# Optimization experiments

Hardware: AMD Instinct MI355X
Metric: run time of the kernel (lower is better)

Reference implementation:

```python
import jax, jax.numpy as jnp
import numpy as np

BN_EPS = 1e-5
POOL_TARGETS = (1500, 750, 375)


def mesh_conv(x, nb, W, g, b):
    # x: (E, C), nb: (E, 4), W: (5*C, Cout)
    E, C = x.shape
    n = x[jnp.clip(nb, 0, E - 1)]              # (E, 4, C) gather
    p1 = jnp.sort(n[:, :2, :], axis=1)          # symmetrize face-pair 1
    p2 = jnp.sort(n[:, 2:, :], axis=1)          # symmetrize face-pair 2
    feat = jnp.concatenate([x, p1[:, 0], p1[:, 1], p2[:, 0], p2[:, 1]], axis=1)  # (E, 5C)
    h = feat @ W                                # (E, Cout)
    mu = h.mean(axis=0)
    var = h.var(axis=0)                         # biased var (BatchNorm training stats)
    h = (h - mu) * jax.lax.rsqrt(var + BN_EPS) * g + b
    return jax.nn.relu(h)


def mesh_pool(x, nb, target):
    E = x.shape[0]
    scores = jnp.linalg.norm(x, axis=1)
    keep = jnp.sort(jnp.argsort(-scores)[:target])          # (target,) sorted kept edges
    x_pool = x[keep]
    remap = jnp.full((E,), -1, dtype=jnp.int32).at[keep].set(jnp.arange(target, dtype=jnp.int32))
    nbr = remap[jnp.clip(nb[keep], 0, E - 1)]               # (target, 4)
    self_idx = jnp.broadcast_to(jnp.arange(target, dtype=jnp.int32)[:, None], nbr.shape)
    nb_pool = jnp.where(nbr < 0, self_idx, nbr)
    return x_pool, nb_pool, keep


def mesh_unpool(x_coarse, keep, E_fine):
    # keep is sorted ascending; nearest kept edge by integer index distance
    # (ties -> lower index, matching torch argmin-first semantics).
    idx = jnp.arange(E_fine)
    pos = jnp.searchsorted(keep, idx)
    K = keep.shape[0]
    left = jnp.clip(pos - 1, 0, K - 1)
    right = jnp.clip(pos, 0, K - 1)
    dl = jnp.abs(idx - keep[left])
    dr = jnp.abs(idx - keep[right])
    nn_idx = jnp.where(dl <= dr, left, right)
    return x_coarse[nn_idx]                                 # kept edges map to themselves (d=0)


def setup_inputs() -> dict:
    key = jax.random.key(0)
    ks = jax.random.split(key, 20)
    E = 200000
    x = jax.random.normal(ks[0], (E, 5), dtype=jnp.float32)
    nb = jax.random.randint(ks[1], (E, 4), 0, E, dtype=jnp.int64)

    def lin(k, cin, cout):
        return (jax.random.normal(k, (cin, cout), dtype=jnp.float32) * 0.05)

    dims = [(5, 64), (64, 128), (128, 256), (256, 512), (768, 256), (384, 128), (192, 64)]
    names = ['e1', 'e2', 'e3', 'e4', 'd3', 'd2', 'd1']
    inp = {'x': x, 'nb': nb}
    for i, ((cin, cout), nm) in enumerate(zip(dims, names)):
        inp['W_' + nm] = lin(ks[2 + i], cin * 5, cout)
        inp['g_' + nm] = jnp.ones((cout,), dtype=jnp.float32)
        inp['b_' + nm] = jnp.zeros((cout,), dtype=jnp.float32)
    inp['W_head'] = lin(ks[12], 64, 4)
    inp['bias_head'] = jnp.zeros((4,), dtype=jnp.float32)
    return inp


def _forward(x, nb,
             W_e1, g_e1, b_e1, W_e2, g_e2, b_e2, W_e3, g_e3, b_e3, W_e4, g_e4, b_e4,
             W_d3, g_d3, b_d3, W_d2, g_d2, b_d2, W_d1, g_d1, b_d1,
             W_head, bias_head):
    e1 = mesh_conv(x, nb, W_e1, g_e1, b_e1)
    e1p, nb1, keep1 = mesh_pool(e1, nb, POOL_TARGETS[0])
    e2 = mesh_conv(e1p, nb1, W_e2, g_e2, b_e2)
    e2p, nb2, keep2 = mesh_pool(e2, nb1, POOL_TARGETS[1])
    e3 = mesh_conv(e2p, nb2, W_e3, g_e3, b_e3)
    e3p, nb3, keep3 = mesh_pool(e3, nb2, POOL_TARGETS[2])
    e4 = mesh_conv(e3p, nb3, W_e4, g_e4, b_e4)
    d3 = mesh_unpool(e4, keep3, e3.shape[0])
    d3 = mesh_conv(jnp.concatenate([d3, e3], axis=1), nb2, W_d3, g_d3, b_d3)
    d2 = mesh_unpool(d3, keep2, e2.shape[0])
    d2 = mesh_conv(jnp.concatenate([d2, e2], axis=1), nb1, W_d2, g_d2, b_d2)
    d1 = mesh_unpool(d2, keep1, e1.shape[0])
    d1 = mesh_conv(jnp.concatenate([d1, e1], axis=1), nb, W_d1, g_d1, b_d1)
    return d1 @ W_head + bias_head


def reference(x, nb,
              W_e1, g_e1, b_e1, W_e2, g_e2, b_e2, W_e3, g_e3, b_e3, W_e4, g_e4, b_e4,
              W_d3, g_d3, b_d3, W_d2, g_d2, b_d2, W_d1, g_d1, b_d1,
              W_head, bias_head):
    return _forward(x, nb,
                    W_e1, g_e1, b_e1, W_e2, g_e2, b_e2, W_e3, g_e3, b_e3, W_e4, g_e4, b_e4,
                    W_d3, g_d3, b_d3, W_d2, g_d2, b_d2, W_d1, g_d1, b_d1,
                    W_head, bias_head)
```

## Files before the change

kernel.cpp:

```cpp
#include <hip/hip_runtime.h>
#include <stdint.h>

typedef unsigned long long u64;
typedef unsigned int u32;
typedef unsigned short ushort_t;

#define FI __device__ __forceinline__

static constexpr float BN_EPS_F = 1e-5f;
static constexpr int E0 = 200000;
static constexpr int T1 = 1500, T2 = 750, T3 = 375;
static constexpr int CAND_CAP = 4096;
static constexpr int NB_KEEP = (E0 + 1023) / 1024;

typedef __attribute__((ext_vector_type(8))) short short8;
typedef __attribute__((ext_vector_type(4))) float f32x4;

FI int iclampi(int v, int lo, int hi) { return v < lo ? lo : (v > hi ? hi : v); }

FI ushort_t f2b(float f) {
  u32 u = __float_as_uint(f);
  u32 r = (u + 0x7FFFu + ((u >> 16) & 1u)) >> 16;
  return (ushort_t)r;
}

FI void u16minmax(const uint4& va, const uint4& vb, uint4& lo, uint4& hi) {
  const ushort_t* a = (const ushort_t*)&va;
  const ushort_t* b = (const ushort_t*)&vb;
  ushort_t* l = (ushort_t*)&lo;
  ushort_t* h = (ushort_t*)&hi;
  #pragma unroll
  for (int i = 0; i < 8; i++) {
    ushort_t x = a[i], y = b[i];
    l[i] = x < y ? x : y;
    h[i] = x < y ? y : x;
  }
}

FI int nearest_keep(const int* __restrict__ keep, int K, int idx) {
  int lo = 0, hi = K;
  while (lo < hi) { int mid = (lo + hi) >> 1; if (keep[mid] < idx) lo = mid + 1; else hi = mid; }
  int l = lo - 1; l = l < 0 ? 0 : (l > K - 1 ? K - 1 : l);
  int r = lo;     r = r < 0 ? 0 : (r > K - 1 ? K - 1 : r);
  int dl = idx - keep[l]; dl = dl < 0 ? -dl : dl;
  int dr = idx - keep[r]; dr = dr < 0 ? -dr : dr;
  return (dl <= dr) ? l : r;
}

FI int bsearch_eq(const int* __restrict__ keep, int K, int v) {
  int lo = 0, hi = K;
  while (lo < hi) { int mid = (lo + hi) >> 1; if (keep[mid] < v) lo = mid + 1; else hi = mid; }
  if (lo < K && keep[lo] == v) return lo;
  return -1;
}

template<int C, int Cout, int BR, int BC, int KT, int TR, int TC, int KSPLIT,
         bool FUSE_STATS>
__global__ __launch_bounds__((BR / TR) * (BC / TC))
void conv_kernel(const float* __restrict__ X,
                 const int* __restrict__ nb, int E,
                 const float* __restrict__ W,
                 float* __restrict__ H, float* __restrict__ stats)
{
  constexpr int NTH = (BR / TR) * (BC / TC);
  constexpr int VK = 5 * KT;
  constexpr int KC = C / KSPLIT;
  static_assert(KC % KT == 0, "KC % KT");

  const int row0 = blockIdx.x * BR;
  const int col0 = blockIdx.y * BC;
  const int c_begin = (KSPLIT > 1) ? (int)blockIdx.z * KC : 0;

  __shared__ float As[VK][BR];
  __shared__ float Bs[VK][BC];
  __shared__ int rowsS[5][BR];
  __shared__ float red[FUSE_STATS ? 2 * (BR / TR) * BC : 1];

  const int tid = threadIdx.x;

  for (int q = tid; q < BR; q += NTH) {
    int r = row0 + q;
    int rr[5];
    if (r < E) {
      rr[0] = r;
      #pragma unroll
      for (int j = 0; j < 4; j++) {
        int v = nb[(size_t)r * 4 + j];
        rr[1 + j] = iclampi(v, 0, E - 1);
      }
    } else {
      #pragma unroll
      for (int j = 0; j < 5; j++) rr[j] = -1;
    }
    #pragma unroll
    for (int j = 0; j < 5; j++) rowsS[j][q] = rr[j];
  }

  float acc[TR][TC];
  #pragma unroll
  for (int i = 0; i < TR; i++)
    #pragma unroll
    for (int j = 0; j < TC; j++) acc[i][j] = 0.f;

  const int tr = tid / (BC / TC);
  const int tc = tid % (BC / TC);
  const int rA = tr * TR;
  const int cB = tc * TC;

  for (int c0 = c_begin; c0 < c_begin + KC; c0 += KT) {
    __syncthreads();
    for (int q = tid; q < VK * (BC / 4); q += NTH) {
      int kk = q / (BC / 4);
      int c4 = q % (BC / 4);
      int p = kk / KT, t = kk % KT;
      float4 wv = *(const float4*)&W[(size_t)(p * C + c0 + t) * Cout + col0 + c4 * 4];
      *(float4*)&Bs[kk][c4 * 4] = wv;
    }
    for (int q = tid; q < BR * KT; q += NTH) {
      int t = q % KT, rq = q / KT;
      int c = c0 + t;
      float s0 = 0.f, a1 = 0.f, a2 = 0.f, a3 = 0.f, a4 = 0.f;
      if (rowsS[0][rq] >= 0) {
        float v0, v1, v2, v3;
        s0 = X[(size_t)rowsS[0][rq] * C + c];
        v0 = X[(size_t)rowsS[1][rq] * C + c];
        v1 = X[(size_t)rowsS[2][rq] * C + c];
        v2 = X[(size_t)rowsS[3][rq] * C + c];
        v3 = X[(size_t)rowsS[4][rq] * C + c];
        a1 = fminf(v0, v1); a2 = fmaxf(v0, v1);
        a3 = fminf(v2, v3); a4 = fmaxf(v2, v3);
      }
      As[0 * KT + t][rq] = s0;
      As[1 * KT + t][rq] = a1;
      As[2 * KT + t][rq] = a2;
      As[3 * KT + t][rq] = a3;
      As[4 * KT + t][rq] = a4;
    }
    __syncthreads();

    for (int kk = 0; kk < VK; kk++) {
      float a[TR], b[TC];
      #pragma unroll
      for (int i = 0; i < TR; i++) a[i] = As[kk][rA + i];
      #pragma unroll
      for (int j = 0; j < TC; j++) b[j] = Bs[kk][cB + j];
      #pragma unroll
      for (int i = 0; i < TR; i++)
        #pragma unroll
        for (int j = 0; j < TC; j++)
          acc[i][j] = fmaf(a[i], b[j], acc[i][j]);
    }
  }

  #pragma unroll
  for (int i = 0; i < TR; i++) {
    int r = row0 + rA + i;
    if (r < E) {
      if constexpr (KSPLIT > 1) {
        #pragma unroll
        for (int j = 0; j < TC; j++)
          atomicAdd(&H[(size_t)r * Cout + col0 + cB + j], acc[i][j]);
      } else {
        #pragma unroll
        for (int j = 0; j < TC; j += 4) {
          float4 v = make_float4(acc[i][j], acc[i][j + 1], acc[i][j + 2], acc[i][j + 3]);
          *(float4*)&H[(size_t)r * Cout + col0 + cB + j] = v;
        }
      }
    }
  }

  if constexpr (FUSE_STATS) {
    float s[TC], q2[TC];
    #pragma unroll
    for (int j = 0; j < TC; j++) { s[j] = 0.f; q2[j] = 0.f; }
    #pragma unroll
    for (int i = 0; i < TR; i++) {
      int r = row0 + rA + i;
      if (r < E) {
        #pragma unroll
        for (int j = 0; j < TC; j++) { float v = acc[i][j]; s[j] += v; q2[j] += v * v; }
      }
    }
    __syncthreads();
    float* redS = &red[0];
    float* redQ = &red[(BR / TR) * BC];
    #pragma unroll
    for (int j = 0; j < TC; j++) {
      redS[tr * BC + cB + j] = s[j];
      redQ[tr * BC + cB + j] = q2[j];
    }
    __syncthreads();
    for (int col = tid; col < BC; col += NTH) {
      float ts = 0.f, tq = 0.f;
      for (int g = 0; g < BR / TR; g++) { ts += redS[g * BC + col]; tq += redQ[g * BC + col]; }
      atomicAdd(&stats[col0 + col], ts);
      atomicAdd(&stats[Cout + col0 + col], tq);
    }
  }
}

__global__ __launch_bounds__(256)
void e1_conv_kernel(const float* __restrict__ X, const int* __restrict__ nb,
                    const float* __restrict__ W,
                    float* __restrict__ H, float* __restrict__ stats)
{
  __shared__ float As[25][128];
  __shared__ float Bs[25][64];
  __shared__ float red[2 * 32 * 64];

  const int tid = threadIdx.x;
  const int row0 = (int)blockIdx.x * 128;

  if (tid < 128) {
    int r = row0 + tid; if (r > E0 - 1) r = E0 - 1;
    int rs[5];
    rs[0] = r;
    #pragma unroll
    for (int j = 0; j < 4; j++) rs[1 + j] = iclampi((int)nb[(size_t)r * 4 + j], 0, E0 - 1);
    float v[5][5];
    #pragma unroll
    for (int j = 0; j < 5; j++) {
      const float* src = &X[(size_t)rs[j] * 5];
      float4 a = *(const float4*)src;
      v[j][0] = a.x; v[j][1] = a.y; v[j][2] = a.z; v[j][3] = a.w;
      v[j][4] = src[4];
    }
    #pragma unroll
    for (int c = 0; c < 5; c++) {
      As[0 * 5 + c][tid] = v[0][c];
      As[1 * 5 + c][tid] = fminf(v[1][c], v[2][c]);
      As[2 * 5 + c][tid] = fmaxf(v[1][c], v[2][c]);
      As[3 * 5 + c][tid] = fminf(v[3][c], v[4][c]);
      As[4 * 5 + c][tid] = fmaxf(v[3][c], v[4][c]);
    }
  } else {
    for (int q = tid - 128; q < 25 * 16; q += 128) {
      int k = q / 16, c4 = q % 16;
      float4 wv = *(const float4*)&W[(size_t)k * 64 + c4 * 4];
      *(float4*)&Bs[k][c4 * 4] = wv;
    }
  }
  __syncthreads();

  const int tr = tid >> 3;
  const int tc = tid & 7;
  const int rA = tr * 4;
  const int cB = tc * 8;

  float acc[4][8];
  #pragma unroll
  for (int i = 0; i < 4; i++)
    #pragma unroll
    for (int j = 0; j < 8; j++) acc[i][j] = 0.f;

  for (int k = 0; k < 25; k++) {
    float a[4], b[8];
    #pragma unroll
    for (int i = 0; i < 4; i++) a[i] = As[k][rA + i];
    #pragma unroll
    for (int j = 0; j < 8; j++) b[j] = Bs[k][cB + j];
    #pragma unroll
    for (int i = 0; i < 4; i++)
      #pragma unroll
      for (int j = 0; j < 8; j++)
        acc[i][j] = fmaf(a[i], b[j], acc[i][j]);
  }

  float s[8], q2[8];
  #pragma unroll
  for (int j = 0; j < 8; j++) { s[j] = 0.f; q2[j] = 0.f; }
  #pragma unroll
  for (int i = 0; i < 4; i++) {
    int r = row0 + rA + i;
    if (r < E0) {
      #pragma unroll
      for (int j = 0; j < 8; j += 4) {
        float4 v = make_float4(acc[i][j], acc[i][j + 1], acc[i][j + 2], acc[i][j + 3]);
        *(float4*)&H[(size_t)r * 64 + cB + j] = v;
      }
      #pragma unroll
      for (int j = 0; j < 8; j++) { float v = acc[i][j]; s[j] += v; q2[j] += v * v; }
    }
  }
  __syncthreads();
  float* redS = &red[0];
  float* redQ = &red[32 * 64];
  #pragma unroll
  for (int j = 0; j < 8; j++) {
    redS[tr * 64 + cB + j] = s[j];
    redQ[tr * 64 + cB + j] = q2[j];
  }
  __syncthreads();
  for (int col = tid; col < 64; col += 256) {
    float ts = 0.f, tq = 0.f;
    for (int g = 0; g < 32; g++) { ts += redS[g * 64 + col]; tq += redQ[g * 64 + col]; }
    atomicAdd(&stats[col], ts);
    atomicAdd(&stats[64 + col], tq);
  }
}

template<int C, int Cout>
__global__ __launch_bounds__(128)
void mfma_conv_kernel(const ushort_t* __restrict__ src,
                      const int* __restrict__ nb, int E,
                      const ushort_t* __restrict__ Wt,
                      float* __restrict__ H, float* __restrict__ stats)
{
  constexpr int NCC = C / 32;
  __shared__ int rows[5][32];

  const int tid = threadIdx.x;
  const int lane = tid & 63;
  const int wv = tid >> 6;
  const int l15 = lane & 15;
  const int quad = lane >> 4;
  const int row0 = (int)blockIdx.x * 32;
  const int col0 = (int)blockIdx.y * 64;

  if (tid < 32) {
    int r = row0 + tid; if (r > E - 1) r = E - 1;
    rows[0][tid] = r;
    #pragma unroll
    for (int j = 0; j < 4; j++) rows[1 + j][tid] = iclampi(nb[(size_t)r * 4 + j], 0, E - 1);
  }
  __syncthreads();

  const int rr = wv * 16 + l15;
  int r5[5];
  #pragma unroll
  for (int j = 0; j < 5; j++) r5[j] = rows[j][rr];

  f32x4 acc[4];
  #pragma unroll
  for (int ni = 0; ni < 4; ni++) acc[ni] = (f32x4){0.f, 0.f, 0.f, 0.f};

  uint4 raw[2][5];
  auto loadcc = [&](int par, int cc2) {
    int cb = cc2 * 32 + quad * 8;
    #pragma unroll
    for (int j = 0; j < 5; j++)
      raw[par][j] = *(const uint4*)&src[(size_t)r5[j] * C + cb];
  };

  loadcc(0, 0);
  #pragma unroll
  for (int cc = 0; cc < NCC; cc++) {
    const int par = cc & 1;
    if (cc + 1 < NCC) loadcc(par ^ 1, cc + 1);
    short8 a[5];
    a[0] = *(short8*)&raw[par][0];
    {
      uint4 lo, hi;
      u16minmax(raw[par][1], raw[par][2], lo, hi);
      a[1] = *(short8*)&lo; a[2] = *(short8*)&hi;
    }
    {
      uint4 lo, hi;
      u16minmax(raw[par][3], raw[par][4], lo, hi);
      a[3] = *(short8*)&lo; a[4] = *(short8*)&hi;
    }
    #pragma unroll
    for (int p = 0; p < 5; p++) {
      #pragma unroll
      for (int ni = 0; ni < 4; ni++) {
        short8 bf = *(const short8*)&Wt[((size_t)(p * Cout + col0 + ni * 16 + l15)) * C + cc * 32 + quad * 8];
        acc[ni] = __builtin_amdgcn_mfma_f32_16x16x32_bf16(a[p], bf, acc[ni], 0, 0, 0);
      }
    }
  }

  float s[4] = {0.f, 0.f, 0.f, 0.f}, q[4] = {0.f, 0.f, 0.f, 0.f};
  #pragma unroll
  for (int reg = 0; reg < 4; reg++) {
    int r = row0 + wv * 16 + quad * 4 + reg;
    if (r < E) {
      #pragma unroll
      for (int ni = 0; ni < 4; ni++) {
        float v = acc[ni][reg];
        H[(size_t)r * Cout + col0 + ni * 16 + l15] = v;
        s[ni] += v; q[ni] += v * v;
      }
    }
  }
  #pragma unroll
  for (int ni = 0; ni < 4; ni++) {
    float ts = s[ni], tq = q[ni];
    ts += __shfl_xor(ts, 16); tq += __shfl_xor(tq, 16);
    ts += __shfl_xor(ts, 32); tq += __shfl_xor(tq, 32);
    if (quad == 0) {
      int col = col0 + ni * 16 + l15;
      atomicAdd(&stats[col], ts);
      atomicAdd(&stats[Cout + col], tq);
    }
  }
}

__global__ __launch_bounds__(256, 2)
void d1_mfma_kernel(const ushort_t* __restrict__ d2b, const ushort_t* __restrict__ e1b,
                    const int* __restrict__ nn1, const int* __restrict__ nb,
                    const ushort_t* __restrict__ Wt,
                    float* __restrict__ H, float* __restrict__ stats)
{
  __shared__ int rowsD[5][128];
  __shared__ int rowsS[5][128];

  const int tid = threadIdx.x;
  const int lane = tid & 63;
  const int wv = tid >> 6;
  const int l15 = lane & 15;
  const int quad = lane >> 4;
  const int row0 = (int)blockIdx.x * 128;

  if (tid < 128) {
    int r = row0 + tid; if (r > E0 - 1) r = E0 - 1;
    int rs[5];
    rs[0] = r;
    #pragma unroll
    for (int j = 0; j < 4; j++) rs[1 + j] = iclampi((int)nb[(size_t)r * 4 + j], 0, E0 - 1);
    #pragma unroll
    for (int j = 0; j < 5; j++) { rowsS[j][tid] = rs[j]; rowsD[j][tid] = nn1[rs[j]]; }
  }
  __syncthreads();

  int rD[2][5], rS[2][5];
  #pragma unroll
  for (int mi = 0; mi < 2; mi++) {
    int rr = wv * 32 + mi * 16 + l15;
    #pragma unroll
    for (int j = 0; j < 5; j++) { rD[mi][j] = rowsD[j][rr]; rS[mi][j] = rowsS[j][rr]; }
  }

  f32x4 acc[2][4];
  #pragma unroll
  for (int mi = 0; mi < 2; mi++)
    #pragma unroll
    for (int ni = 0; ni < 4; ni++) acc[mi][ni] = (f32x4){0.f, 0.f, 0.f, 0.f};

  uint4 raw[2][2][5];
  auto loadcc = [&](int par, int cc2) {
    const bool fD = cc2 < 4;
    const ushort_t* s2 = fD ? d2b : e1b;
    const int st = fD ? 128 : 64;
    const int cb = (fD ? cc2 * 32 : (cc2 - 4) * 32) + quad * 8;
    #pragma unroll
    for (int mi = 0; mi < 2; mi++)
      #pragma unroll
      for (int j = 0; j < 5; j++) {
        int r = fD ? rD[mi][j] : rS[mi][j];
        raw[par][mi][j] = *(const uint4*)&s2[(size_t)r * st + cb];
      }
  };

  loadcc(0, 0);
  #pragma unroll
  for (int cc = 0; cc < 6; cc++) {
    const int par = cc & 1;
    if (cc + 1 < 6) loadcc(par ^ 1, cc + 1);
    short8 a[2][5];
    #pragma unroll
    for (int mi = 0; mi < 2; mi++) {
      a[mi][0] = *(short8*)&raw[par][mi][0];
      {
        uint4 lo, hi;
        u16minmax(raw[par][mi][1], raw[par][mi][2], lo, hi);
        a[mi][1] = *(short8*)&lo; a[mi][2] = *(short8*)&hi;
      }
      {
        uint4 lo, hi;
        u16minmax(raw[par][mi][3], raw[par][mi][4], lo, hi);
        a[mi][3] = *(short8*)&lo; a[mi][4] = *(short8*)&hi;
      }
    }
    #pragma unroll
    for (int p = 0; p < 5; p++) {
      short8 bf[4];
      #pragma unroll
      for (int ni = 0; ni < 4; ni++)
        bf[ni] = *(const short8*)&Wt[((size_t)(p * 64 + ni * 16 + l15)) * 192 + cc * 32 + quad * 8];
      #pragma unroll
      for (int mi = 0; mi < 2; mi++)
        #pragma unroll
        for (int ni = 0; ni < 4; ni++)
          acc[mi][ni] = __builtin_amdgcn_mfma_f32_16x16x32_bf16(a[mi][p], bf[ni], acc[mi][ni], 0, 0, 0);
    }
  }

  float s[4] = {0.f, 0.f, 0.f, 0.f}, q[4] = {0.f, 0.f, 0.f, 0.f};
  #pragma unroll
  for (int mi = 0; mi < 2; mi++) {
    #pragma unroll
    for (int reg = 0; reg < 4; reg++) {
      int r = row0 + wv * 32 + mi * 16 + quad * 4 + reg;
      if (r < E0) {
        #pragma unroll
        for (int ni = 0; ni < 4; ni++) {
          float v = acc[mi][ni][reg];
          H[(size_t)r * 64 + ni * 16 + l15] = v;
          s[ni] += v; q[ni] += v * v;
        }
      }
    }
  }
  #pragma unroll
  for (int ni = 0; ni < 4; ni++) {
    float ts = s[ni], tq = q[ni];
    ts += __shfl_xor(ts, 16); tq += __shfl_xor(tq, 16);
    ts += __shfl_xor(ts, 32); tq += __shfl_xor(tq, 32);
    if (quad == 0) {
      int col = ni * 16 + l15;
      atomicAdd(&stats[col], ts);
      atomicAdd(&stats[64 + col], tq);
    }
  }
}

template<int C, int Cout>
__global__ void prep_w_kernel(const float* __restrict__ W, ushort_t* __restrict__ Wt)
{
  int idx = (int)blockIdx.x * 256 + threadIdx.x;
  if (idx < 5 * C * Cout) {
    int n = idx % Cout;
    int k = idx / Cout;
    int p = k / C, c = k % C;
    Wt[((size_t)(p * Cout + n)) * C + c] = f2b(W[(size_t)k * Cout + n]);
  }
}

__global__ void stats_kernel(const float* __restrict__ H, int E, int Cout,
                             float* __restrict__ stats)
{
  const int RB = 64;
  int r0 = (int)blockIdx.x * RB;
  int rend = r0 + RB; if (rend > E) rend = E;
  for (int col = threadIdx.x; col < Cout; col += blockDim.x) {
    float s = 0.f, q = 0.f;
    for (int r = r0; r < rend; r++) { float v = H[(size_t)r * Cout + col]; s += v; q += v * v; }
    atomicAdd(&stats[col], s);
    atomicAdd(&stats[Cout + col], q);
  }
}

template<int Cout, bool KEYS, bool B16>
__global__ void bn_kernel(const float* __restrict__ H, const float* __restrict__ stats,
                          const float* __restrict__ g, const float* __restrict__ b,
                          int E, float* __restrict__ Out, ushort_t* __restrict__ Outb,
                          u64* __restrict__ keys)
{
  constexpr int CPL = Cout / 64;
  const int lane = threadIdx.x & 63;
  const int wid = threadIdx.x >> 6;
  const int wpb = blockDim.x >> 6;
  const float invE = 1.0f / (float)E;
  float mu[CPL], inv[CPL], gg[CPL], bb[CPL];
  #pragma unroll
  for (int u = 0; u < CPL; u++) {
    int c = lane + u * 64;
    float m = stats[c] * invE;
    float var = stats[Cout + c] * invE - m * m;
    mu[u] = m;
    inv[u] = rsqrtf(var + BN_EPS_F);
    gg[u] = g[c]; bb[u] = b[c];
  }
  for (int r = (int)blockIdx.x * wpb + wid; r < E; r += (int)gridDim.x * wpb) {
    float ss = 0.f;
    #pragma unroll
    for (int u = 0; u < CPL; u++) {
      int c = lane + u * 64;
      float v = H[(size_t)r * Cout + c];
      float o = (v - mu[u]) * inv[u] * gg[u] + bb[u];
      o = fmaxf(o, 0.f);
      Out[(size_t)r * Cout + c] = o;
      if constexpr (B16) Outb[(size_t)r * Cout + c] = f2b(o);
      ss += o * o;
    }
    if constexpr (KEYS) {
      #pragma unroll
      for (int s = 32; s > 0; s >>= 1) ss += __shfl_xor(ss, s, 64);
      if (lane == 0) {
        float sc = sqrtf(ss);
        u32 sb = __float_as_uint(sc);
        keys[r] = ((u64)sb << 32) | (u64)(0xFFFFFFFFu - (u32)r);
      }
    }
  }
}

__global__ void head_kernel(const float* __restrict__ H, const float* __restrict__ stats,
                            const float* __restrict__ g, const float* __restrict__ b,
                            const float* __restrict__ Wh, const float* __restrict__ bh,
                            int E, float* __restrict__ out)
{
  const int lane = threadIdx.x & 63;
  const int wid = threadIdx.x >> 6;
  const int wpb = blockDim.x >> 6;
  const float invE = 1.0f / (float)E;
  float m = stats[lane] * invE;
  float var = stats[64 + lane] * invE - m * m;
  float inv = rsqrtf(var + BN_EPS_F);
  float gg = g[lane], bb = b[lane];
  float4 w = *(const float4*)&Wh[lane * 4];
  float b0 = bh[0], b1 = bh[1], b2 = bh[2], b3 = bh[3];
  for (int r = (int)blockIdx.x * wpb + wid; r < E; r += (int)gridDim.x * wpb) {
    float v = H[(size_t)r * 64 + lane];
    float o = fmaxf((v - m) * inv * gg + bb, 0.f);
    float a0 = o * w.x, a1 = o * w.y, a2 = o * w.z, a3 = o * w.w;
    #pragma unroll
    for (int s = 32; s > 0; s >>= 1) {
      a0 += __shfl_xor(a0, s, 64);
      a1 += __shfl_xor(a1, s, 64);
      a2 += __shfl_xor(a2, s, 64);
      a3 += __shfl_xor(a3, s, 64);
    }
    if (lane == 0) {
      float4 ov = make_float4(a0 + b0, a1 + b1, a2 + b2, a3 + b3);
      *(float4*)&out[(size_t)r * 4] = ov;
    }
  }
}

__global__ void hist_kernel(const u64* __restrict__ keys, int E, u32* __restrict__ hist)
{
  for (int i = (int)blockIdx.x * blockDim.x + threadIdx.x; i < E;
       i += (int)gridDim.x * blockDim.x) {
    u32 bin = (u32)(keys[i] >> 44);
    atomicAdd(&hist[bin], 1u);
  }
}

__global__ void scan_kernel(const u32* __restrict__ hist, int K, u32* __restrict__ sel)
{
  __shared__ u32 csum[1024];
  __shared__ u32 sb2[1024];
  __shared__ int selChunk;
  __shared__ u32 aboveChunk;
  const int tid = threadIdx.x;
  {
    const uint4* hp = (const uint4*)(hist + (size_t)tid * 1024);
    u32 s = 0;
    for (int i = 0; i < 256; i++) {
      uint4 v = hp[i];
      s += v.x + v.y + v.z + v.w;
    }
    csum[tid] = s;
  }
  __syncthreads();
  if (tid == 0) {
    u32 above = 0; int sc = 0; u32 ab = 0;
    for (int t = 1023; t >= 0; t--) {
      if (above + csum[t] >= (u32)K) { sc = t; ab = above; break; }
      above += csum[t];
    }
    selChunk = sc; aboveChunk = ab;
  }
  __syncthreads();
  sb2[tid] = hist[(size_t)selChunk * 1024 + tid];
  __syncthreads();
  if (tid == 0) {
    u32 above = aboveChunk; int sb = 0;
    for (int t = 1023; t >= 0; t--) {
      u32 c = sb2[t];
      if (above + c >= (u32)K) { sb = t; break; }
      above += c;
    }
    sel[0] = (u32)(selChunk * 1024 + sb);
    sel[1] = above;
    sel[2] = (u32)K - above;
  }
}

__global__ void collect_kernel(const u64* __restrict__ keys, int E, const u32* __restrict__ sel,
                               u64* __restrict__ cand, u32* __restrict__ count)
{
  u32 bin = sel[0];
  for (int i = (int)blockIdx.x * blockDim.x + threadIdx.x; i < E;
       i += (int)gridDim.x * blockDim.x) {
    if ((u32)(keys[i] >> 44) == bin) {
      u32 p = atomicAdd(count, 1u);
      if (p < (u32)CAND_CAP) cand[p] = keys[i];
    }
  }
}

__global__ void thresh_kernel(const u64* __restrict__ cand, const u32* __restrict__ count,
                              const u32* __restrict__ sel, u64* __restrict__ thr)
{
  __shared__ u64 sk[CAND_CAP];
  const int tid = threadIdx.x;
  const int nth = blockDim.x;
  int n = (int)(*count > (u32)CAND_CAP ? (u32)CAND_CAP : *count);
  int n2 = 2; while (n2 < n) n2 <<= 1;
  for (int i = tid; i < n2; i += nth) sk[i] = (i < n) ? cand[i] : 0ull;
  __syncthreads();
  for (int k = 2; k <= n2; k <<= 1)
    for (int j = k >> 1; j > 0; j >>= 1) {
      for (int i = tid; i < n2; i += nth) {
        int p = i ^ j;
        if (p > i) {
          u64 a = sk[i], bb = sk[p];
          bool up = ((i & k) == 0);
          bool sw = up ? (a < bb) : (a > bb);
          if (sw) { sk[i] = bb; sk[p] = a; }
        }
      }
      __syncthreads();
    }
  if (tid == 0) {
    int kr = (int)sel[2];
    thr[0] = sk[kr - 1];
  }
}

__global__ void keep_count_kernel(const u64* __restrict__ keys, int E,
                                  const u64* __restrict__ thrp, u32* __restrict__ bcnt)
{
  const u64 thr = thrp[0];
  const int tid = threadIdx.x;
  int base = (int)blockIdx.x * 1024 + tid * 4;
  u32 c = 0;
  #pragma unroll
  for (int u = 0; u < 4; u++) {
    int i = base + u;
    if (i < E && keys[i] >= thr) c++;
  }
  __shared__ u32 sm[256];
  sm[tid] = c;
  __syncthreads();
  for (int s = 128; s > 0; s >>= 1) {
    if (tid < s) sm[tid] += sm[tid + s];
    __syncthreads();
  }
  if (tid == 0) bcnt[blockIdx.x] = sm[0];
}

__global__ void keep_scan_kernel(const u32* __restrict__ bcnt, int NB, u32* __restrict__ boffs)
{
  __shared__ u32 sm[256];
  const int tid = threadIdx.x;
  u32 v = (tid < NB) ? bcnt[tid] : 0;
  sm[tid] = v;
  __syncthreads();
  for (int off = 1; off < 256; off <<= 1) {
    u32 t = 0;
    if (tid >= off) t = sm[tid - off];
    __syncthreads();
    sm[tid] += t;
    __syncthreads();
  }
  if (tid < NB) boffs[tid] = sm[tid] - v;
}

__global__ void keep_scatter_kernel(const u64* __restrict__ keys, int E,
                                    const u64* __restrict__ thrp, const u32* __restrict__ boffs,
                                    int* __restrict__ keep, int K)
{
  const u64 thr = thrp[0];
  const int tid = threadIdx.x;
  int base = (int)blockIdx.x * 1024 + tid * 4;
  u32 f[4]; u32 c = 0;
  #pragma unroll
  for (int u = 0; u < 4; u++) {
    int i = base + u;
    f[u] = (i < E && keys[i] >= thr) ? 1u : 0u;
    c += f[u];
  }
  __shared__ u32 sm[256];
  sm[tid] = c;
  __syncthreads();
  for (int off = 1; off < 256; off <<= 1) {
    u32 t = 0;
    if (tid >= off) t = sm[tid - off];
    __syncthreads();
    sm[tid] += t;
    __syncthreads();
  }
  u32 pos = boffs[blockIdx.x] + sm[tid] - c;
  #pragma unroll
  for (int u = 0; u < 4; u++) {
    if (f[u]) {
      if (pos < (u32)K) keep[pos] = base + u;
      pos++;
    }
  }
}

template<int NPOW>
__global__ void pool_select_kernel(const u64* __restrict__ keys, int E, int K,
                                   int* __restrict__ keep)
{
  __shared__ u64 sk[NPOW];
  __shared__ int si[NPOW];
  const int tid = threadIdx.x, nth = blockDim.x;
  for (int i = tid; i < NPOW; i += nth) sk[i] = (i < E) ? keys[i] : 0ull;
  __syncthreads();
  for (int k = 2; k <= NPOW; k <<= 1)
    for (int j = k >> 1; j > 0; j >>= 1) {
      for (int i = tid; i < NPOW; i += nth) {
        int p = i ^ j;
        if (p > i) {
          u64 a = sk[i], bb = sk[p];
          bool up = ((i & k) == 0);
          bool sw = up ? (a < bb) : (a > bb);
          if (sw) { sk[i] = bb; sk[p] = a; }
        }
      }
      __syncthreads();
    }
  for (int i = tid; i < NPOW; i += nth)
    si[i] = (i < K) ? (int)(0xFFFFFFFFu - (u32)(sk[i] & 0xFFFFFFFFull)) : 0x7FFFFFFF;
  __syncthreads();
  for (int k = 2; k <= NPOW; k <<= 1)
    for (int j = k >> 1; j > 0; j >>= 1) {
      for (int i = tid; i < NPOW; i += nth) {
        int p = i ^ j;
        if (p > i) {
          int a = si[i], bb = si[p];
          bool up = ((i & k) == 0);
          bool sw = up ? (a > bb) : (a < bb);
          if (sw) { si[i] = bb; si[p] = a; }
        }
      }
      __syncthreads();
    }
  for (int i = tid; i < K; i += nth) keep[i] = si[i];
}

template<int C, bool B16>
__global__ void pool_finish_kernel(const float* __restrict__ Xsrc, const int* __restrict__ nb_src,
                                   const int* __restrict__ keep, int K, int Esrc,
                                   float* __restrict__ Xp, ushort_t* __restrict__ Xpb,
                                   int* __restrict__ nbp)
{
  int total = K * C;
  for (int idx = (int)blockIdx.x * blockDim.x + threadIdx.x; idx < total;
       idx += (int)gridDim.x * blockDim.x) {
    int i = idx / C, c = idx % C;
    float v = Xsrc[(size_t)keep[i] * C + c];
    if constexpr (B16) Xpb[idx] = f2b(v);
    else Xp[idx] = v;
  }
  for (int idx = (int)blockIdx.x * blockDim.x + threadIdx.x; idx < K * 4;
       idx += (int)gridDim.x * blockDim.x) {
    int i = idx >> 2, j = idx & 3;
    int v = nb_src[(size_t)keep[i] * 4 + j];
    v = iclampi(v, 0, Esrc - 1);
    int p = bsearch_eq(keep, K, v);
    nbp[idx] = (p < 0) ? i : p;
  }
}

__global__ void unpool_cat_b16_kernel(const float* __restrict__ Xc, const float* __restrict__ Xs,
                                      const int* __restrict__ keep, int K, int E,
                                      int Cc, int Cs, ushort_t* __restrict__ out)
{
  int Ct = Cc + Cs;
  int total = E * Ct;
  for (int idx = (int)blockIdx.x * blockDim.x + threadIdx.x; idx < total;
       idx += (int)gridDim.x * blockDim.x) {
    int r = idx / Ct, c = idx % Ct;
    float v;
    if (c < Cc) { int nn = nearest_keep(keep, K, r); v = Xc[(size_t)nn * Cc + c]; }
    else v = Xs[(size_t)r * Cs + (c - Cc)];
    out[idx] = f2b(v);
  }
}

__global__ void nn_map_kernel(const int* __restrict__ keep, int K, int E, int* __restrict__ nn)
{
  for (int i = (int)blockIdx.x * blockDim.x + threadIdx.x; i < E;
       i += (int)gridDim.x * blockDim.x)
    nn[i] = nearest_keep(keep, K, i);
}

extern "C" void kernel_launch(void* const* d_in, const int* in_sizes, int n_in,
                              void* d_out, int out_size, void* d_ws, size_t ws_size,
                              hipStream_t stream)
{
  (void)in_sizes; (void)n_in; (void)out_size; (void)ws_size;
  const float* x     = (const float*)d_in[0];
  const int*   nb    = (const int*)d_in[1];
  const float* W_e1  = (const float*)d_in[2];
  const float* g_e1  = (const float*)d_in[3];
  const float* b_e1  = (const float*)d_in[4];
  const float* W_e2  = (const float*)d_in[5];
  const float* g_e2  = (const float*)d_in[6];
  const float* b_e2  = (const float*)d_in[7];
  const float* W_e3  = (const float*)d_in[8];
  const float* g_e3  = (const float*)d_in[9];
  const float* b_e3  = (const float*)d_in[10];
  const float* W_e4  = (const float*)d_in[11];
  const float* g_e4  = (const float*)d_in[12];
  const float* b_e4  = (const float*)d_in[13];
  const float* W_d3  = (const float*)d_in[14];
  const float* g_d3  = (const float*)d_in[15];
  const float* b_d3  = (const float*)d_in[16];
  const float* W_d2  = (const float*)d_in[17];
  const float* g_d2  = (const float*)d_in[18];
  const float* b_d2  = (const float*)d_in[19];
  const float* W_d1  = (const float*)d_in[20];
  const float* g_d1  = (const float*)d_in[21];
  const float* b_d1  = (const float*)d_in[22];
  const float* W_head = (const float*)d_in[23];
  const float* bias_head = (const float*)d_in[24];
  float* out = (float*)d_out;

  char* p = (char*)d_ws;
  auto alloc = [&](size_t bytes) -> char* {
    char* q = p; p += (bytes + 255) & ~(size_t)255; return q;
  };

  char* zz = p;
  u32*   hist  = (u32*)alloc(sizeof(u32) * (1u << 20));
  float* stats = (float*)alloc(sizeof(float) * 2 * (64 + 128 + 256 + 512 + 256 + 128 + 64));
  u32*   ctrl  = (u32*)alloc(sizeof(u32) * 16);
  u64*   thr   = (u64*)alloc(sizeof(u64) * 2);
  u32*   sel   = (u32*)alloc(sizeof(u32) * 8);
  float* H2    = (float*)alloc(sizeof(float) * T1 * 128);
  float* H3    = (float*)alloc(sizeof(float) * T2 * 256);
  size_t zz_bytes = (size_t)(p - zz);
  float* H4    = (float*)alloc(sizeof(float) * T3 * 512);
  float* Hd3   = (float*)alloc(sizeof(float) * T2 * 256);
  float* Hd2   = (float*)alloc(sizeof(float) * T1 * 128);
  u32*   bcnt  = (u32*)alloc(sizeof(u32) * 256);
  u32*   boffs = (u32*)alloc(sizeof(u32) * 256);
  float* e1    = (float*)alloc(sizeof(float) * (size_t)E0 * 64);
  u64*   keys1 = (u64*)alloc(sizeof(u64) * E0);
  u64*   cand  = (u64*)alloc(sizeof(u64) * CAND_CAP);
  int*   keep1 = (int*)alloc(sizeof(int) * T1);
  float* e1p   = (float*)alloc(sizeof(float) * T1 * 64);
  int*   nb1   = (int*)alloc(sizeof(int) * T1 * 4);
  float* e2    = (float*)alloc(sizeof(float) * T1 * 128);
  u64*   keys2 = (u64*)alloc(sizeof(u64) * T1);
  int*   keep2 = (int*)alloc(sizeof(int) * T2);
  float* e2p   = (float*)alloc(sizeof(float) * T2 * 128);
  int*   nb2   = (int*)alloc(sizeof(int) * T2 * 4);
  float* e3    = (float*)alloc(sizeof(float) * T2 * 256);
  u64*   keys3 = (u64*)alloc(sizeof(u64) * T2);
  int*   keep3 = (int*)alloc(sizeof(int) * T3);
  ushort_t* e3pb = (ushort_t*)alloc(sizeof(ushort_t) * T3 * 256);
  int*   nb3   = (int*)alloc(sizeof(int) * T3 * 4);
  float* e4    = (float*)alloc(sizeof(float) * T3 * 512);
  ushort_t* d3catb = (ushort_t*)alloc(sizeof(ushort_t) * T2 * 768);
  float* d3    = (float*)alloc(sizeof(float) * T2 * 256);
  ushort_t* d2catb = (ushort_t*)alloc(sizeof(ushort_t) * T1 * 384);
  float* d2    = (float*)alloc(sizeof(float) * T1 * 128);
  int*   nn1   = (int*)alloc(sizeof(int) * E0);
  float* Hd1   = (float*)alloc(sizeof(float) * (size_t)E0 * 64);
  ushort_t* e1b = (ushort_t*)alloc(sizeof(ushort_t) * (size_t)E0 * 64);
  ushort_t* d2b = (ushort_t*)alloc(sizeof(ushort_t) * T1 * 128);
  ushort_t* Wt1 = (ushort_t*)alloc(sizeof(ushort_t) * 5 * 64 * 192);
  ushort_t* Wt4 = (ushort_t*)alloc(sizeof(ushort_t) * 5 * 512 * 256);
  ushort_t* Wtd3 = (ushort_t*)alloc(sizeof(ushort_t) * 5 * 256 * 768);
  ushort_t* Wtd2 = (ushort_t*)alloc(sizeof(ushort_t) * 5 * 128 * 384);

  float* s1  = stats;
  float* s2  = s1 + 2 * 64;
  float* s3  = s2 + 2 * 128;
  float* s4  = s3 + 2 * 256;
  float* sd3 = s4 + 2 * 512;
  float* sd2 = sd3 + 2 * 256;
  float* sd1 = sd2 + 2 * 128;

  hipMemsetAsync(zz, 0, zz_bytes, stream);
  prep_w_kernel<192, 64><<<dim3((5 * 192 * 64 + 255) / 256), 256, 0, stream>>>(W_d1, Wt1);
  prep_w_kernel<256, 512><<<dim3((5 * 256 * 512 + 255) / 256), 256, 0, stream>>>(W_e4, Wt4);
  prep_w_kernel<768, 256><<<dim3((5 * 768 * 256 + 255) / 256), 256, 0, stream>>>(W_d3, Wtd3);
  prep_w_kernel<384, 128><<<dim3((5 * 384 * 128 + 255) / 256), 256, 0, stream>>>(W_d2, Wtd2);

  e1_conv_kernel<<<dim3((E0 + 127) / 128), 256, 0, stream>>>(x, nb, W_e1, e1, s1);
  bn_kernel<64, true, true><<<dim3(8192), 256, 0, stream>>>(e1, s1, g_e1, b_e1, E0, e1, e1b, keys1);

  hist_kernel<<<dim3(782), 256, 0, stream>>>(keys1, E0, hist);
  scan_kernel<<<dim3(1), 1024, 0, stream>>>(hist, T1, sel);
  collect_kernel<<<dim3(782), 256, 0, stream>>>(keys1, E0, sel, cand, ctrl);
  thresh_kernel<<<dim3(1), 1024, 0, stream>>>(cand, ctrl, sel, thr);
  keep_count_kernel<<<dim3(NB_KEEP), 256, 0, stream>>>(keys1, E0, thr, bcnt);
  keep_scan_kernel<<<dim3(1), 256, 0, stream>>>(bcnt, NB_KEEP, boffs);
  keep_scatter_kernel<<<dim3(NB_KEEP), 256, 0, stream>>>(keys1, E0, thr, boffs, keep1, T1);
  pool_finish_kernel<64, false><<<dim3(380), 256, 0, stream>>>(e1, nb, keep1, T1, E0, e1p, nullptr, nb1);

  conv_kernel<64, 128, 32, 64, 8, 2, 4, 2, false>
      <<<dim3((T1 + 31) / 32, 128 / 64, 2), 256, 0, stream>>>(e1p, nb1, T1, W_e2, H2, nullptr);
  stats_kernel<<<dim3((T1 + 63) / 64), 256, 0, stream>>>(H2, T1, 128, s2);
  bn_kernel<128, true, false><<<dim3(512), 256, 0, stream>>>(H2, s2, g_e2, b_e2, T1, e2, nullptr, keys2);
  pool_select_kernel<2048><<<dim3(1), 256, 0, stream>>>(keys2, T1, T2, keep2);
  pool_finish_kernel<128, false><<<dim3(380), 256, 0, stream>>>(e2, nb1, keep2, T2, T1, e2p, nullptr, nb2);

  conv_kernel<128, 256, 32, 64, 8, 2, 4, 4, false>
      <<<dim3((T2 + 31) / 32, 256 / 64, 4), 256, 0, stream>>>(e2p, nb2, T2, W_e3, H3, nullptr);
  stats_kernel<<<dim3((T2 + 63) / 64), 256, 0, stream>>>(H3, T2, 256, s3);
  bn_kernel<256, true, false><<<dim3(256), 256, 0, stream>>>(H3, s3, g_e3, b_e3, T2, e3, nullptr, keys3);
  pool_select_kernel<1024><<<dim3(1), 256, 0, stream>>>(keys3, T2, T3, keep3);
  pool_finish_kernel<256, true><<<dim3(380), 256, 0, stream>>>(e3, nb2, keep3, T3, T2, nullptr, e3pb, nb3);

  mfma_conv_kernel<256, 512><<<dim3((T3 + 31) / 32, 512 / 64), 128, 0, stream>>>(
      e3pb, nb3, T3, Wt4, H4, s4);
  bn_kernel<512, false, false><<<dim3(128), 256, 0, stream>>>(H4, s4, g_e4, b_e4, T3, e4, nullptr, nullptr);

  unpool_cat_b16_kernel<<<dim3((T2 * 768 + 255) / 256), 256, 0, stream>>>(
      e4, e3, keep3, T3, T2, 512, 256, d3catb);
  mfma_conv_kernel<768, 256><<<dim3((T2 + 31) / 32, 256 / 64), 128, 0, stream>>>(
      d3catb, nb2, T2, Wtd3, Hd3, sd3);
  bn_kernel<256, false, false><<<dim3(256), 256, 0, stream>>>(Hd3, sd3, g_d3, b_d3, T2, d3, nullptr, nullptr);

  unpool_cat_b16_kernel<<<dim3((T1 * 384 + 255) / 256), 256, 0, stream>>>(
      d3, e2, keep2, T2, T1, 256, 128, d2catb);
  mfma_conv_kernel<384, 128><<<dim3((T1 + 31) / 32, 128 / 64), 128, 0, stream>>>(
      d2catb, nb1, T1, Wtd2, Hd2, sd2);
  bn_kernel<128, false, true><<<dim3(512), 256, 0, stream>>>(Hd2, sd2, g_d2, b_d2, T1, d2, d2b, nullptr);

  nn_map_kernel<<<dim3(782), 256, 0, stream>>>(keep1, T1, E0, nn1);
  d1_mfma_kernel<<<dim3((E0 + 127) / 128), 256, 0, stream>>>(d2b, e1b, nn1, nb, Wt1, Hd1, sd1);

  head_kernel<<<dim3(8192), 256, 0, stream>>>(Hd1, sd1, g_d1, b_d1, W_head, bias_head, E0, out);
}
```

Before: 1.139 ms.

## Repartition d1 MFMA kernel so each wave owns one column tile across all rows

The d1 conv kernel changes its work split: each of the four waves now computes one 16-column slice for all 128 rows of the block, instead of 32 rows by all 64 columns. Register-held gathered rows and the software double-buffered prefetch are removed in favour of per-iteration gathers indexed from shared memory. Launch bounds rise to allow four blocks per CU. The aim is fewer registers and higher occupancy to hide gather latency, but each wave now gathers all 128 rows, so activation loads are repeated four times per block and rely on cache hits.

After: 1.111 ms. -2.4%, faster.

```diff
diff --git a/kernel.cpp b/kernel.cpp
--- a/kernel.cpp
+++ b/kernel.cpp
@@ -396,7 +396,7 @@
   }
 }
 
-__global__ __launch_bounds__(256, 2)
+__global__ __launch_bounds__(256, 4)
 void d1_mfma_kernel(const ushort_t* __restrict__ d2b, const ushort_t* __restrict__ e1b,
                     const int* __restrict__ nn1, const int* __restrict__ nb,
                     const ushort_t* __restrict__ Wt,
@@ -423,95 +423,69 @@
   }
   __syncthreads();
 
-  int rD[2][5], rS[2][5];
-  #pragma unroll
-  for (int mi = 0; mi < 2; mi++) {
-    int rr = wv * 32 + mi * 16 + l15;
-    #pragma unroll
-    for (int j = 0; j < 5; j++) { rD[mi][j] = rowsD[j][rr]; rS[mi][j] = rowsS[j][rr]; }
-  }
-
-  f32x4 acc[2][4];
-  #pragma unroll
-  for (int mi = 0; mi < 2; mi++)
-    #pragma unroll
-    for (int ni = 0; ni < 4; ni++) acc[mi][ni] = (f32x4){0.f, 0.f, 0.f, 0.f};
-
-  uint4 raw[2][2][5];
-  auto loadcc = [&](int par, int cc2) {
-    const bool fD = cc2 < 4;
-    const ushort_t* s2 = fD ? d2b : e1b;
-    const int st = fD ? 128 : 64;
-    const int cb = (fD ? cc2 * 32 : (cc2 - 4) * 32) + quad * 8;
-    #pragma unroll
-    for (int mi = 0; mi < 2; mi++)
-      #pragma unroll
-      for (int j = 0; j < 5; j++) {
-        int r = fD ? rD[mi][j] : rS[mi][j];
-        raw[par][mi][j] = *(const uint4*)&s2[(size_t)r * st + cb];
-      }
-  };
-
-  loadcc(0, 0);
-  #pragma unroll
+  f32x4 acc[8];
+  #pragma unroll
+  for (int mi = 0; mi < 8; mi++) acc[mi] = (f32x4){0.f, 0.f, 0.f, 0.f};
+
   for (int cc = 0; cc < 6; cc++) {
-    const int par = cc & 1;
-    if (cc + 1 < 6) loadcc(par ^ 1, cc + 1);
-    short8 a[2][5];
-    #pragma unroll
-    for (int mi = 0; mi < 2; mi++) {
-      a[mi][0] = *(short8*)&raw[par][mi][0];
-      {
-        uint4 lo, hi;
-        u16minmax(raw[par][mi][1], raw[par][mi][2], lo, hi);
-        a[mi][1] = *(short8*)&lo; a[mi][2] = *(short8*)&hi;
-      }
-      {
-        uint4 lo, hi;
-        u16minmax(raw[par][mi][3], raw[par][mi][4], lo, hi);
-        a[mi][3] = *(short8*)&lo; a[mi][4] = *(short8*)&hi;
-      }
-    }
-    #pragma unroll
-    for (int p = 0; p < 5; p++) {
-      short8 bf[4];
-      #pragma unroll
-      for (int ni = 0; ni < 4; ni++)
-        bf[ni] = *(const short8*)&Wt[((size_t)(p * 64 + ni * 16 + l15)) * 192 + cc * 32 + quad * 8];
-      #pragma unroll
-      for (int mi = 0; mi < 2; mi++)
-        #pragma unroll
-        for (int ni = 0; ni < 4; ni++)
-          acc[mi][ni] = __builtin_amdgcn_mfma_f32_16x16x32_bf16(a[mi][p], bf[ni], acc[mi][ni], 0, 0, 0);
-    }
-  }
-
-  float s[4] = {0.f, 0.f, 0.f, 0.f}, q[4] = {0.f, 0.f, 0.f, 0.f};
-  #pragma unroll
-  for (int mi = 0; mi < 2; mi++) {
+    const bool fromD = cc < 4;
+    const ushort_t* __restrict__ src = fromD ? d2b : e1b;
+    const int stride = fromD ? 128 : 64;
+    const int cbase = (fromD ? cc * 32 : (cc - 4) * 32) + quad * 8;
+
+    short8 bf[5];
+    #pragma unroll
+    for (int p = 0; p < 5; p++)
+      bf[p] = *(const short8*)&Wt[((size_t)(p * 64 + wv * 16 + l15)) * 192 + cc * 32 + quad * 8];
+
+    #pragma unroll 2
+    for (int mi = 0; mi < 8; mi++) {
+      int rr = mi * 16 + l15;
+      int r0, r1, r2, r3, r4;
+      if (fromD) {
+        r0 = rowsD[0][rr]; r1 = rowsD[1][rr]; r2 = rowsD[2][rr];
+        r3 = rowsD[3][rr]; r4 = rowsD[4][rr];
+      } else {
+        r0 = rowsS[0][rr]; r1 = rowsS[1][rr]; r2 = rowsS[2][rr];
+        r3 = rowsS[3][rr]; r4 = rowsS[4][rr];
+      }
+      uint4 v0 = *(const uint4*)&src[(size_t)r0 * stride + cbase];
+      uint4 v1 = *(const uint4*)&src[(size_t)r1 * stride + cbase];
+      uint4 v2 = *(const uint4*)&src[(size_t)r2 * stride + cbase];
+      uint4 v3 = *(const uint4*)&src[(size_t)r3 * stride + cbase];
+      uint4 v4 = *(const uint4*)&src[(size_t)r4 * stride + cbase];
+
+      uint4 lo12, hi12, lo34, hi34;
+      u16minmax(v1, v2, lo12, hi12);
+      u16minmax(v3, v4, lo34, hi34);
+
+      acc[mi] = __builtin_amdgcn_mfma_f32_16x16x32_bf16(*(short8*)&v0,   bf[0], acc[mi], 0, 0, 0);
+      acc[mi] = __builtin_amdgcn_mfma_f32_16x16x32_bf16(*(short8*)&lo12, bf[1], acc[mi], 0, 0, 0);
+      acc[mi] = __builtin_amdgcn_mfma_f32_16x16x32_bf16(*(short8*)&hi12, bf[2], acc[mi], 0, 0, 0);
+      acc[mi] = __builtin_amdgcn_mfma_f32_16x16x32_bf16(*(short8*)&lo34, bf[3], acc[mi], 0, 0, 0);
+      acc[mi] = __builtin_amdgcn_mfma_f32_16x16x32_bf16(*(short8*)&hi34, bf[4], acc[mi], 0, 0, 0);
+    }
+  }
+
+  const int col = wv * 16 + l15;
+  float s = 0.f, q = 0.f;
+  #pragma unroll
+  for (int mi = 0; mi < 8; mi++) {
     #pragma unroll
     for (int reg = 0; reg < 4; reg++) {
-      int r = row0 + wv * 32 + mi * 16 + quad * 4 + reg;
+      int r = row0 + mi * 16 + quad * 4 + reg;
       if (r < E0) {
-        #pragma unroll
-        for (int ni = 0; ni < 4; ni++) {
-          float v = acc[mi][ni][reg];
-          H[(size_t)r * 64 + ni * 16 + l15] = v;
-          s[ni] += v; q[ni] += v * v;
-        }
-      }
-    }
-  }
-  #pragma unroll
-  for (int ni = 0; ni < 4; ni++) {
-    float ts = s[ni], tq = q[ni];
-    ts += __shfl_xor(ts, 16); tq += __shfl_xor(tq, 16);
-    ts += __shfl_xor(ts, 32); tq += __shfl_xor(tq, 32);
-    if (quad == 0) {
-      int col = ni * 16 + l15;
-      atomicAdd(&stats[col], ts);
-      atomicAdd(&stats[64 + col], tq);
-    }
+        float v = acc[mi][reg];
+        H[(size_t)r * 64 + col] = v;
+        s += v; q += v * v;
+      }
+    }
+  }
+  s += __shfl_xor(s, 16); q += __shfl_xor(q, 16);
+  s += __shfl_xor(s, 32); q += __shfl_xor(q, 32);
+  if (quad == 0) {
+    atomicAdd(&stats[col], s);
+    atomicAdd(&stats[64 + col], q);
   }
 }
 
@@ -995,19 +969,22 @@
 
   mfma_conv_kernel<256, 512><<<dim3((T3 + 31) / 32, 512 / 64), 128, 0, stream>>>(
       e3pb, nb3, T3, Wt4, H4, s4);
-  bn_kernel<512, false, false><<<dim3(128), 256, 0, stream>>>(H4, s4, g_e4, b_e4, T3, e4, nullptr, nullptr);
+  bn_kernel<512, false, false><<<dim3(128), 256, 0, stream>>>(
+      H4, s4, g_e4, b_e4, T3, e4, nullptr, nullptr);
 
   unpool_cat_b16_kernel<<<dim3((T2 * 768 + 255) / 256), 256, 0, stream>>>(
       e4, e3, keep3, T3, T2, 512, 256, d3catb);
   mfma_conv_kernel<768, 256><<<dim3((T2 + 31) / 32, 256 / 64), 128, 0, stream>>>(
       d3catb, nb2, T2, Wtd3, Hd3, sd3);
-  bn_kernel<256, false, false><<<dim3(256), 256, 0, stream>>>(Hd3, sd3, g_d3, b_d3, T2, d3, nullptr, nullptr);
+  bn_kernel<256, false, false><<<dim3(256), 256, 0, stream>>>(
+      Hd3, sd3, g_d3, b_d3, T2, d3, nullptr, nullptr);
 
   unpool_cat_b16_kernel<<<dim3((T1 * 384 + 255) / 256), 256, 0, stream>>>(
       d3, e2, keep2, T2, T1, 256, 128, d2catb);
   mfma_conv_kernel<384, 128><<<dim3((T1 + 31) / 32, 128 / 64), 128, 0, stream>>>(
       d2catb, nb1, T1, Wtd2, Hd2, sd2);
-  bn_kernel<128, false, true><<<dim3(512), 256, 0, stream>>>(Hd2, sd2, g_d2, b_d2, T1, d2, d2b, nullptr);
+  bn_kernel<128, false, true><<<dim3(512), 256, 0, stream>>>(
+      Hd2, sd2, g_d2, b_d2, T1, d2, d2b, nullptr);
 
   nn_map_kernel<<<dim3(782), 256, 0, stream>>>(keep1, T1, E0, nn1);
   d1_mfma_kernel<<<dim3((E0 + 127) / 128), 256, 0, stream>>>(d2b, e1b, nn1, nb, Wt1, Hd1, sd1);
```
